# Performance work log

Hardware: AMD Instinct MI355X
Metric: run time of the kernel (lower is better)

## Reference

```python
import jax, jax.numpy as jnp
import numpy as np

HIDDEN = 1024
EMB = HIDDEN // 2          # embedding_dim = hidden_dim // 2
NUM_OPS = 8
BATCH = 16384


def setup_inputs() -> dict:
    key = jax.random.key(0)
    ks = jax.random.split(key, 8)
    x = jax.random.normal(ks[0], (BATCH, HIDDEN), dtype=jnp.float32)
    sampled_ops = jax.random.randint(ks[1], (BATCH,), 0, NUM_OPS, dtype=jnp.int32)
    op_emb = jax.random.normal(ks[2], (NUM_OPS, EMB), dtype=jnp.float32) * 0.02
    # per-expert 2-layer MLP params (Linear stored as [in, out] for x @ W)
    s1 = 1.0 / np.sqrt(HIDDEN + EMB)
    s2 = 1.0 / np.sqrt(HIDDEN)
    W1 = jax.random.uniform(ks[3], (NUM_OPS, HIDDEN + EMB, HIDDEN), jnp.float32, -s1, s1)
    b1 = jax.random.uniform(ks[4], (NUM_OPS, HIDDEN), jnp.float32, -s1, s1)
    W2 = jax.random.uniform(ks[5], (NUM_OPS, HIDDEN, HIDDEN), jnp.float32, -s2, s2)
    b2 = jax.random.uniform(ks[6], (NUM_OPS, HIDDEN), jnp.float32, -s2, s2)
    return {"x": x, "sampled_ops": sampled_ops, "op_emb": op_emb,
            "W1": W1, "b1": b1, "W2": W2, "b2": b2}


def reference(x, sampled_ops, op_emb, W1, b1, W2, b2):
    # gather per-token operator embedding and augment input
    emb = jnp.take(op_emb, sampled_ops, axis=0)            # [B, EMB]
    x_aug = jnp.concatenate([x, emb], axis=-1)             # [B, H+EMB]
    num_ops = W1.shape[0]
    out = jnp.zeros_like(x)
    # loop over the small fixed expert set; mask-combine per token
    for o in range(num_ops):
        h = jax.nn.relu(x_aug @ W1[o] + b1[o])             # [B, H]
        y = jax.nn.relu(h @ W2[o] + b2[o])                 # [B, H]
        mask = (sampled_ops == o)[:, None]
        out = out + jnp.where(mask, y, 0.0)
    return out
```

## Files before the change

kernel.cpp:

```cpp
#include <hip/hip_runtime.h>
#include <hip/hip_bf16.h>

#define BATCH 16384
#define HID   1024
#define EMBD  512
#define NOPS  8
#define MAXT  136
#define CNTS  16

typedef __attribute__((ext_vector_type(8))) short bf16x8;
typedef __attribute__((ext_vector_type(4))) float f32x4;

__device__ __forceinline__ unsigned short f2bf(float f) {
  unsigned int u = __float_as_uint(f);
  u += 0x7FFF + ((u >> 16) & 1);
  return (unsigned short)(u >> 16);
}

__device__ __forceinline__ unsigned int pk2(float a, float b) {
  __hip_bfloat162 t = __float22bfloat162_rn(make_float2(a, b));
  return *(unsigned int*)(&t);
}

__device__ __forceinline__ void lds_load16(void* lds, const void* g) {
  __builtin_amdgcn_global_load_lds(
      (const __attribute__((address_space(1))) unsigned int*)g,
      (__attribute__((address_space(3))) unsigned int*)lds, 16, 0, 0);
}

__device__ __forceinline__ void decode_bid(int bid, int& g, int& nx) {
  g = 17 * (bid & 7) + (bid >> 6);
  nx = (bid >> 3) & 7;
}

__device__ __forceinline__ void w_prep_tile(const float* __restrict__ W,
                                            short* __restrict__ Wp,
                                            int ks, int nx, int tid) {
  int n = tid & 127, kh = tid >> 7;
  const float* src = W + (size_t)(ks * 32 + kh * 16) * 1024 + nx * 128 + n;
  float v[16];
#pragma unroll
  for (int kk = 0; kk < 16; ++kk) v[kk] = src[(size_t)kk * 1024];
  uint4 a, b;
  a.x = pk2(v[0], v[1]);  a.y = pk2(v[2], v[3]);
  a.z = pk2(v[4], v[5]);  a.w = pk2(v[6], v[7]);
  b.x = pk2(v[8], v[9]);  b.y = pk2(v[10], v[11]);
  b.z = pk2(v[12], v[13]); b.w = pk2(v[14], v[15]);
  uint4* dst = (uint4*)(Wp + (size_t)n * 32);
  dst[kh * 2] = a;
  dst[kh * 2 + 1] = b;
}

__global__ void bucket_ce_k(const int* __restrict__ ops, int* __restrict__ cnt,
                            int* __restrict__ idx, const float* __restrict__ W1,
                            const float* __restrict__ emb,
                            const float* __restrict__ b1, float* __restrict__ ce) {
  int bid = blockIdx.x;
  int tid = threadIdx.x;
  if (bid < 128) {
    int e = bid >> 4, kp = bid & 15;
    int n = tid * 4;
    const float* Wc = W1 + (size_t)e * 1536 * 1024 + (size_t)(1024 + kp * 32) * 1024 + n;
    const float* ee = emb + e * EMBD + kp * 32;
    float4 a = make_float4(0.f, 0.f, 0.f, 0.f);
#pragma unroll
    for (int kk = 0; kk < 32; ++kk) {
      float s = ee[kk];
      float4 r = *(const float4*)(Wc + (size_t)kk * 1024);
      a.x += s * r.x; a.y += s * r.y; a.z += s * r.z; a.w += s * r.w;
    }
    if (kp == 0) {
      float4 b = *(const float4*)(b1 + e * HID + n);
      a.x += b.x; a.y += b.y; a.z += b.z; a.w += b.w;
    }
    float* d = ce + e * HID + n;
    atomicAdd(d + 0, a.x); atomicAdd(d + 1, a.y);
    atomicAdd(d + 2, a.z); atomicAdd(d + 3, a.w);
    return;
  }
  __shared__ int wcnt[4][NOPS];
  __shared__ int wbase[4][NOPS];
  int lane = tid & 63, w = tid >> 6;
  int t = (bid - 128) * 256 + tid;
  int op = ops[t];
  unsigned long long msave = 0;
#pragma unroll
  for (int o = 0; o < NOPS; ++o) {
    unsigned long long mm = __ballot(op == o);
    if (op == o) msave = mm;
    if (lane == o) wcnt[w][o] = __popcll(mm);
  }
  __syncthreads();
  if (tid < NOPS) {
    int c0 = wcnt[0][tid], c1 = wcnt[1][tid], c2 = wcnt[2][tid], c3 = wcnt[3][tid];
    int base = atomicAdd(&cnt[tid * CNTS], c0 + c1 + c2 + c3);
    wbase[0][tid] = base;
    wbase[1][tid] = base + c0;
    wbase[2][tid] = base + c0 + c1;
    wbase[3][tid] = base + c0 + c1 + c2;
  }
  __syncthreads();
  int pre = __popcll(msave & ((1ull << lane) - 1ull));
  idx[op * BATCH + wbase[w][op] + pre] = t;
}

__global__ void schedule_k(const int* __restrict__ cnt, int* __restrict__ desc,
                           int* __restrict__ ntp, int* __restrict__ idx) {
  if (threadIdx.x == 0) {
    int n = 0;
    for (int e = 0; e < NOPS; ++e) {
      int c = cnt[e * CNTS];
      for (int t = 0; t < c; t += 128) { desc[2 * n] = e; desc[2 * n + 1] = t; ++n; }
    }
    *ntp = n;
  }
  for (int e = 0; e < NOPS; ++e) {
    int c = cnt[e * CNTS];
    int cp = (c + 127) & ~127;
    for (int p = c + (int)threadIdx.x; p < cp; p += 256) idx[e * BATCH + p] = 0;
  }
}

__global__ void prep_k(const float* __restrict__ x,
                       const int* __restrict__ idx, const int* __restrict__ desc,
                       const int* __restrict__ ntp, short* __restrict__ Ap,
                       const float* __restrict__ W1, short* __restrict__ W1p) {
  int bid = blockIdx.x;
  int tid = threadIdx.x;
  if (bid >= 8 * MAXT) {
    int b = bid - 8 * MAXT;
    int e = b / 256; int r = b % 256; int nx = r / 32, ks = r % 32;
    w_prep_tile(W1 + (size_t)e * 1536 * 1024,
                W1p + ((size_t)(e * 8 + nx) * 32 + ks) * 4096, ks, nx, tid);
    return;
  }
  __shared__ int toks[128];
  int g = bid >> 3, kx = bid & 7;
  if (g >= *ntp) return;
  int e = desc[2 * g], rs = desc[2 * g + 1];
  if (tid < 128) toks[tid] = idx[e * BATCH + rs + tid];
  __syncthreads();
  int r = tid >> 1, ah = tid & 1;
  int tok = toks[r];
  short* dst0 = Ap + (size_t)g * 32 * 4096;
#pragma unroll
  for (int kk = 0; kk < 4; ++kk) {
    int ks = kx * 4 + kk;
    const float* src = x + (size_t)tok * HID + ks * 32 + ah * 16;
    float4 f0 = ((const float4*)src)[0];
    float4 f1 = ((const float4*)src)[1];
    float4 f2v = ((const float4*)src)[2];
    float4 f3 = ((const float4*)src)[3];
    uint4 p0 = make_uint4(pk2(f0.x, f0.y), pk2(f0.z, f0.w), pk2(f1.x, f1.y), pk2(f1.z, f1.w));
    uint4 p1 = make_uint4(pk2(f2v.x, f2v.y), pk2(f2v.z, f2v.w), pk2(f3.x, f3.y), pk2(f3.z, f3.w));
    short* dst = dst0 + ks * 4096 + r * 32 + ah * 16;
    ((uint4*)dst)[0] = p0;
    ((uint4*)dst)[1] = p1;
  }
}

__global__ __launch_bounds__(256) void gemm1_w2_k(
    const short* __restrict__ Ap, const float* __restrict__ ce,
    const short* __restrict__ W1p, unsigned short* __restrict__ hp,
    const int* __restrict__ desc, const int* __restrict__ ntp,
    const float* __restrict__ W2, short* __restrict__ W2p) {
  int bid = blockIdx.x;
  int tid = threadIdx.x;
  if (bid >= 8 * MAXT) {
    int b = bid - 8 * MAXT;
    int e = b / 256; int r = b % 256; int nx = r / 32, ks = r % 32;
    w_prep_tile(W2 + (size_t)e * 1024 * 1024,
                W2p + ((size_t)(e * 8 + nx) * 32 + ks) * 4096, ks, nx, tid);
    return;
  }
  int g, nx;
  decode_bid(bid, g, nx);
  if (g >= *ntp) return;
  int e = desc[2 * g];

  __shared__ __align__(16) char smem[16384];
  short* lA = (short*)smem;
  short* lB = (short*)(smem + 8192);

  int lane = tid & 63, w = tid >> 6;
  int wm = w >> 1, wn = w & 1;
  int fr = lane & 15, fq = lane >> 4;

  const char* Asrc = (const char*)Ap + (size_t)g * 32 * 8192;
  const char* Bsrc = (const char*)W1p + (size_t)(e * 8 + nx) * 32 * 8192;

  f32x4 acc[4][4] = {};

  for (int ks = 0; ks < 32; ++ks) {
    const char* as = Asrc + ks * 8192;
    const char* bs = Bsrc + ks * 8192;
    lds_load16(smem + w * 1024, as + w * 1024 + lane * 16);
    lds_load16(smem + 4096 + w * 1024, as + 4096 + w * 1024 + lane * 16);
    lds_load16(smem + 8192 + w * 1024, bs + w * 1024 + lane * 16);
    lds_load16(smem + 12288 + w * 1024, bs + 4096 + w * 1024 + lane * 16);
    __syncthreads();

    bf16x8 af[4], bfr[4];
#pragma unroll
    for (int i = 0; i < 4; ++i)
      af[i] = *(const bf16x8*)&lA[(wm * 64 + i * 16 + fr) * 32 + fq * 8];
#pragma unroll
    for (int j = 0; j < 4; ++j)
      bfr[j] = *(const bf16x8*)&lB[(wn * 64 + j * 16 + fr) * 32 + fq * 8];
#pragma unroll
    for (int i = 0; i < 4; ++i)
#pragma unroll
      for (int j = 0; j < 4; ++j)
        acc[i][j] = __builtin_amdgcn_mfma_f32_16x16x32_bf16(af[i], bfr[j], acc[i][j], 0, 0, 0);
    __syncthreads();
  }

  float bias[4];
#pragma unroll
  for (int j = 0; j < 4; ++j)
    bias[j] = ce[e * HID + nx * 128 + wn * 64 + j * 16 + fr];

  unsigned short* ls = (unsigned short*)smem;
  int lr = lane >> 2;
#pragma unroll
  for (int i = 0; i < 4; ++i) {
    __syncthreads();
#pragma unroll
    for (int j = 0; j < 4; ++j)
#pragma unroll
      for (int rg = 0; rg < 4; ++rg) {
        float v = acc[i][j][rg] + bias[j];
        v = v > 0.f ? v : 0.f;
        ls[w * 1024 + (fq * 4 + rg) * 64 + j * 16 + fr] = f2bf(v);
      }
    __syncthreads();
    int R = wm * 64 + i * 16 + lr;
#pragma unroll
    for (int s = 0; s < 2; ++s) {
      int ch = (lane & 3) + s * 4;
      int ks2 = nx * 4 + wn * 2 + (ch >> 2);
      uint4 val = *(const uint4*)&ls[w * 1024 + lr * 64 + ch * 8];
      *(uint4*)(hp + ((size_t)(g * 32 + ks2) * 128 + R) * 32 + (ch & 3) * 8) = val;
    }
  }
}

__global__ __launch_bounds__(256) void gemm2_k(
    const unsigned short* __restrict__ hp, const float* __restrict__ b2,
    const short* __restrict__ W2p, float* __restrict__ out,
    const int* __restrict__ idx, const int* __restrict__ cnt,
    const int* __restrict__ desc, const int* __restrict__ ntp) {
  int g, nx;
  decode_bid(blockIdx.x, g, nx);
  if (g >= *ntp) return;
  int e = desc[2 * g], rs = desc[2 * g + 1];
  int ce2 = cnt[e * CNTS];

  __shared__ __align__(16) char smem[16384];
  __shared__ int toks[128];
  short* lA = (short*)smem;
  short* lB = (short*)(smem + 8192);

  int tid = threadIdx.x, lane = tid & 63, w = tid >> 6;
  int wm = w >> 1, wn = w & 1;
  int fr = lane & 15, fq = lane >> 4;

  if (tid < 128) toks[tid] = idx[e * BATCH + rs + tid];

  const char* Asrc = (const char*)hp + (size_t)g * 32 * 8192;
  const char* Bsrc = (const char*)W2p + (size_t)(e * 8 + nx) * 32 * 8192;

  f32x4 acc[4][4] = {};

  for (int ks = 0; ks < 32; ++ks) {
    const char* as = Asrc + ks * 8192;
    const char* bs = Bsrc + ks * 8192;
    lds_load16(smem + w * 1024, as + w * 1024 + lane * 16);
    lds_load16(smem + 4096 + w * 1024, as + 4096 + w * 1024 + lane * 16);
    lds_load16(smem + 8192 + w * 1024, bs + w * 1024 + lane * 16);
    lds_load16(smem + 12288 + w * 1024, bs + 4096 + w * 1024 + lane * 16);
    __syncthreads();

    bf16x8 af[4], bfr[4];
#pragma unroll
    for (int i = 0; i < 4; ++i)
      af[i] = *(const bf16x8*)&lA[(wm * 64 + i * 16 + fr) * 32 + fq * 8];
#pragma unroll
    for (int j = 0; j < 4; ++j)
      bfr[j] = *(const bf16x8*)&lB[(wn * 64 + j * 16 + fr) * 32 + fq * 8];
#pragma unroll
    for (int i = 0; i < 4; ++i)
#pragma unroll
      for (int j = 0; j < 4; ++j)
        acc[i][j] = __builtin_amdgcn_mfma_f32_16x16x32_bf16(af[i], bfr[j], acc[i][j], 0, 0, 0);
    __syncthreads();
  }

  float bias[4];
#pragma unroll
  for (int j = 0; j < 4; ++j)
    bias[j] = b2[e * HID + nx * 128 + wn * 64 + j * 16 + fr];

  float* lsf = (float*)smem;
  int lr = lane >> 2;
#pragma unroll
  for (int i = 0; i < 4; ++i) {
    __syncthreads();
#pragma unroll
    for (int j = 0; j < 4; ++j)
#pragma unroll
      for (int rg = 0; rg < 4; ++rg) {
        float v = acc[i][j][rg] + bias[j];
        lsf[w * 1024 + (fq * 4 + rg) * 64 + j * 16 + fr] = v > 0.f ? v : 0.f;
      }
    __syncthreads();
    int R = wm * 64 + i * 16 + lr;
    if (R < ce2 - rs) {
      float* orow = out + (size_t)toks[R] * HID + nx * 128 + wn * 64;
#pragma unroll
      for (int s = 0; s < 4; ++s) {
        int ch = (lane & 3) + s * 4;
        *(float4*)(orow + ch * 4) = *(const float4*)&lsf[w * 1024 + lr * 64 + ch * 4];
      }
    }
  }
}


extern "C" void kernel_launch(void* const* d_in, const int* in_sizes, int n_in,
                              void* d_out, int out_size, void* d_ws, size_t ws_size,
                              hipStream_t stream) {
  const float* x   = (const float*)d_in[0];
  const int*   ops = (const int*)d_in[1];
  const float* emb = (const float*)d_in[2];
  const float* W1  = (const float*)d_in[3];
  const float* b1  = (const float*)d_in[4];
  const float* W2  = (const float*)d_in[5];
  const float* b2  = (const float*)d_in[6];
  float* out = (float*)d_out;

  char* ws = (char*)d_ws;
  int* cnt  = (int*)(ws + 0);
  float* ce = (float*)(ws + 512);
  int* ntp  = (int*)(ws + 33280);
  int* desc = (int*)(ws + 33344);
  int* idx  = (int*)(ws + 36864);
  short* W1p = (short*)(ws + 561152);
  short* W2p = (short*)(ws + 17338368);
  unsigned short* hp = (unsigned short*)(ws + 34115584);
  short* Ap = (short*)(ws + 69767168);

  hipMemsetAsync(ws, 0, 33280, stream);
  bucket_ce_k<<<128 + 64, 256, 0, stream>>>(ops, cnt, idx, W1, emb, b1, ce);
  schedule_k<<<1, 256, 0, stream>>>(cnt, desc, ntp, idx);
  prep_k<<<8 * MAXT + 2048, 256, 0, stream>>>(x, idx, desc, ntp, Ap, W1, W1p);
  gemm1_w2_k<<<8 * MAXT + 2048, 256, 0, stream>>>(Ap, ce, W1p, hp, desc, ntp, W2, W2p);
  gemm2_k<<<8 * MAXT, 256, 0, stream>>>(hp, b2, W2p, out, idx, cnt, desc, ntp);
}
```

Before: 303.4 us.

## Fuse token gather and bf16 conversion into GEMM1, drop prep kernel

Removes the separate prep kernel that gathered x rows and wrote a packed bf16 A buffer. GEMM1 now loads the gathered fp32 rows directly, converts them in registers and stores them to LDS, prefetching the next k-slice. W1 packing moves into the bucketing kernel. The packed tile layout changes to a k-quarter-major form, and the epilogue LDS staging gets an XOR swizzle to cut bank conflicts. Schedule descriptor writes are parallelised across threads. Each of the 8 column blocks now re-reads and re-converts the same x rows, which adds redundant global traffic and conversion work.

```diff
diff --git a/kernel.cpp b/kernel.cpp
--- a/kernel.cpp
+++ b/kernel.cpp
@@ -46,19 +46,28 @@
   a.z = pk2(v[4], v[5]);  a.w = pk2(v[6], v[7]);
   b.x = pk2(v[8], v[9]);  b.y = pk2(v[10], v[11]);
   b.z = pk2(v[12], v[13]); b.w = pk2(v[14], v[15]);
-  uint4* dst = (uint4*)(Wp + (size_t)n * 32);
-  dst[kh * 2] = a;
-  dst[kh * 2 + 1] = b;
+  uint4* dst = (uint4*)Wp;
+  dst[(2 * kh) * 128 + n]     = a;
+  dst[(2 * kh + 1) * 128 + n] = b;
 }
 
 __global__ void bucket_ce_k(const int* __restrict__ ops, int* __restrict__ cnt,
                             int* __restrict__ idx, const float* __restrict__ W1,
                             const float* __restrict__ emb,
-                            const float* __restrict__ b1, float* __restrict__ ce) {
+                            const float* __restrict__ b1, float* __restrict__ ce,
+                            short* __restrict__ W1p) {
   int bid = blockIdx.x;
   int tid = threadIdx.x;
-  if (bid < 128) {
-    int e = bid >> 4, kp = bid & 15;
+  if (bid >= 192) {
+    int b = bid - 192;
+    int e = b / 256; int rr = b % 256; int nx = rr / 32, ks = rr % 32;
+    w_prep_tile(W1 + (size_t)e * 1536 * 1024,
+                W1p + ((size_t)(e * 8 + nx) * 32 + ks) * 4096, ks, nx, tid);
+    return;
+  }
+  if (bid >= 64) {
+    int cb = bid - 64;
+    int e = cb >> 4, kp = cb & 15;
     int n = tid * 4;
     const float* Wc = W1 + (size_t)e * 1536 * 1024 + (size_t)(1024 + kp * 32) * 1024 + n;
     const float* ee = emb + e * EMBD + kp * 32;
@@ -81,7 +90,7 @@
   __shared__ int wcnt[4][NOPS];
   __shared__ int wbase[4][NOPS];
   int lane = tid & 63, w = tid >> 6;
-  int t = (bid - 128) * 256 + tid;
+  int t = bid * 256 + tid;
   int op = ops[t];
   unsigned long long msave = 0;
 #pragma unroll
@@ -106,69 +115,40 @@
 
 __global__ void schedule_k(const int* __restrict__ cnt, int* __restrict__ desc,
                            int* __restrict__ ntp, int* __restrict__ idx) {
-  if (threadIdx.x == 0) {
+  __shared__ int base[NOPS + 1];
+  int tid = threadIdx.x;
+  if (tid == 0) {
     int n = 0;
-    for (int e = 0; e < NOPS; ++e) {
-      int c = cnt[e * CNTS];
-      for (int t = 0; t < c; t += 128) { desc[2 * n] = e; desc[2 * n + 1] = t; ++n; }
-    }
+    for (int e = 0; e < NOPS; ++e) { base[e] = n; n += (cnt[e * CNTS] + 127) >> 7; }
+    base[NOPS] = n;
     *ntp = n;
+  }
+  __syncthreads();
+  for (int e = 0; e < NOPS; ++e) {
+    int b0 = base[e], nt = base[e + 1] - b0;
+    for (int t = tid; t < nt; t += 256) {
+      desc[2 * (b0 + t)] = e;
+      desc[2 * (b0 + t) + 1] = t * 128;
+    }
   }
   for (int e = 0; e < NOPS; ++e) {
     int c = cnt[e * CNTS];
     int cp = (c + 127) & ~127;
-    for (int p = c + (int)threadIdx.x; p < cp; p += 256) idx[e * BATCH + p] = 0;
-  }
-}
-
-__global__ void prep_k(const float* __restrict__ x,
-                       const int* __restrict__ idx, const int* __restrict__ desc,
-                       const int* __restrict__ ntp, short* __restrict__ Ap,
-                       const float* __restrict__ W1, short* __restrict__ W1p) {
+    for (int p = c + tid; p < cp; p += 256) idx[e * BATCH + p] = 0;
+  }
+}
+
+__global__ __launch_bounds__(256) void gemm1_w2_k(
+    const float* __restrict__ x, const int* __restrict__ idx,
+    const float* __restrict__ ce, const short* __restrict__ W1p,
+    unsigned short* __restrict__ hp, const int* __restrict__ desc,
+    const int* __restrict__ ntp, const float* __restrict__ W2,
+    short* __restrict__ W2p) {
   int bid = blockIdx.x;
   int tid = threadIdx.x;
   if (bid >= 8 * MAXT) {
     int b = bid - 8 * MAXT;
-    int e = b / 256; int r = b % 256; int nx = r / 32, ks = r % 32;
-    w_prep_tile(W1 + (size_t)e * 1536 * 1024,
-                W1p + ((size_t)(e * 8 + nx) * 32 + ks) * 4096, ks, nx, tid);
-    return;
-  }
-  __shared__ int toks[128];
-  int g = bid >> 3, kx = bid & 7;
-  if (g >= *ntp) return;
-  int e = desc[2 * g], rs = desc[2 * g + 1];
-  if (tid < 128) toks[tid] = idx[e * BATCH + rs + tid];
-  __syncthreads();
-  int r = tid >> 1, ah = tid & 1;
-  int tok = toks[r];
-  short* dst0 = Ap + (size_t)g * 32 * 4096;
-#pragma unroll
-  for (int kk = 0; kk < 4; ++kk) {
-    int ks = kx * 4 + kk;
-    const float* src = x + (size_t)tok * HID + ks * 32 + ah * 16;
-    float4 f0 = ((const float4*)src)[0];
-    float4 f1 = ((const float4*)src)[1];
-    float4 f2v = ((const float4*)src)[2];
-    float4 f3 = ((const float4*)src)[3];
-    uint4 p0 = make_uint4(pk2(f0.x, f0.y), pk2(f0.z, f0.w), pk2(f1.x, f1.y), pk2(f1.z, f1.w));
-    uint4 p1 = make_uint4(pk2(f2v.x, f2v.y), pk2(f2v.z, f2v.w), pk2(f3.x, f3.y), pk2(f3.z, f3.w));
-    short* dst = dst0 + ks * 4096 + r * 32 + ah * 16;
-    ((uint4*)dst)[0] = p0;
-    ((uint4*)dst)[1] = p1;
-  }
-}
-
-__global__ __launch_bounds__(256) void gemm1_w2_k(
-    const short* __restrict__ Ap, const float* __restrict__ ce,
-    const short* __restrict__ W1p, unsigned short* __restrict__ hp,
-    const int* __restrict__ desc, const int* __restrict__ ntp,
-    const float* __restrict__ W2, short* __restrict__ W2p) {
-  int bid = blockIdx.x;
-  int tid = threadIdx.x;
-  if (bid >= 8 * MAXT) {
-    int b = bid - 8 * MAXT;
-    int e = b / 256; int r = b % 256; int nx = r / 32, ks = r % 32;
+    int e = b / 256; int rr = b % 256; int nx = rr / 32, ks = rr % 32;
     w_prep_tile(W2 + (size_t)e * 1024 * 1024,
                 W2p + ((size_t)(e * 8 + nx) * 32 + ks) * 4096, ks, nx, tid);
     return;
@@ -176,37 +156,51 @@
   int g, nx;
   decode_bid(bid, g, nx);
   if (g >= *ntp) return;
-  int e = desc[2 * g];
+  int e = desc[2 * g], rs = desc[2 * g + 1];
 
   __shared__ __align__(16) char smem[16384];
+  __shared__ int toks[128];
   short* lA = (short*)smem;
   short* lB = (short*)(smem + 8192);
 
   int lane = tid & 63, w = tid >> 6;
   int wm = w >> 1, wn = w & 1;
   int fr = lane & 15, fq = lane >> 4;
-
-  const char* Asrc = (const char*)Ap + (size_t)g * 32 * 8192;
+  int ar = tid >> 1, ah = tid & 1;
+
+  if (tid < 128) toks[tid] = idx[e * BATCH + rs + tid];
+  __syncthreads();
+  const float* xrow = x + (size_t)toks[ar] * HID + ah * 16;
   const char* Bsrc = (const char*)W1p + (size_t)(e * 8 + nx) * 32 * 8192;
 
   f32x4 acc[4][4] = {};
+  float4 fa0 = ((const float4*)xrow)[0];
+  float4 fa1 = ((const float4*)xrow)[1];
+  float4 fa2 = ((const float4*)xrow)[2];
+  float4 fa3 = ((const float4*)xrow)[3];
 
   for (int ks = 0; ks < 32; ++ks) {
-    const char* as = Asrc + ks * 8192;
     const char* bs = Bsrc + ks * 8192;
-    lds_load16(smem + w * 1024, as + w * 1024 + lane * 16);
-    lds_load16(smem + 4096 + w * 1024, as + 4096 + w * 1024 + lane * 16);
     lds_load16(smem + 8192 + w * 1024, bs + w * 1024 + lane * 16);
     lds_load16(smem + 12288 + w * 1024, bs + 4096 + w * 1024 + lane * 16);
-    __syncthreads();
-
+    uint4 p0 = make_uint4(pk2(fa0.x, fa0.y), pk2(fa0.z, fa0.w),
+                          pk2(fa1.x, fa1.y), pk2(fa1.z, fa1.w));
+    uint4 p1 = make_uint4(pk2(fa2.x, fa2.y), pk2(fa2.z, fa2.w),
+                          pk2(fa3.x, fa3.y), pk2(fa3.z, fa3.w));
+    *(uint4*)&lA[((2 * ah) * 128 + ar) * 8] = p0;
+    *(uint4*)&lA[((2 * ah + 1) * 128 + ar) * 8] = p1;
+    __syncthreads();
+    if (ks < 31) {
+      const float4* src = (const float4*)(xrow + (ks + 1) * 32);
+      fa0 = src[0]; fa1 = src[1]; fa2 = src[2]; fa3 = src[3];
+    }
     bf16x8 af[4], bfr[4];
 #pragma unroll
     for (int i = 0; i < 4; ++i)
-      af[i] = *(const bf16x8*)&lA[(wm * 64 + i * 16 + fr) * 32 + fq * 8];
+      af[i] = *(const bf16x8*)&lA[(fq * 128 + wm * 64 + i * 16 + fr) * 8];
 #pragma unroll
     for (int j = 0; j < 4; ++j)
-      bfr[j] = *(const bf16x8*)&lB[(wn * 64 + j * 16 + fr) * 32 + fq * 8];
+      bfr[j] = *(const bf16x8*)&lB[(fq * 128 + wn * 64 + j * 16 + fr) * 8];
 #pragma unroll
     for (int i = 0; i < 4; ++i)
 #pragma unroll
@@ -220,7 +214,6 @@
   for (int j = 0; j < 4; ++j)
     bias[j] = ce[e * HID + nx * 128 + wn * 64 + j * 16 + fr];
 
-  unsigned short* ls = (unsigned short*)smem;
   int lr = lane >> 2;
 #pragma unroll
   for (int i = 0; i < 4; ++i) {
@@ -231,16 +224,22 @@
       for (int rg = 0; rg < 4; ++rg) {
         float v = acc[i][j][rg] + bias[j];
         v = v > 0.f ? v : 0.f;
-        ls[w * 1024 + (fq * 4 + rg) * 64 + j * 16 + fr] = f2bf(v);
+        int row16 = fq * 4 + rg;
+        int off = w * 2048 + row16 * 128 + (j * 16 + fr) * 2;
+        off ^= (row16 & 1) << 6;
+        *(unsigned short*)(smem + off) = f2bf(v);
       }
     __syncthreads();
     int R = wm * 64 + i * 16 + lr;
 #pragma unroll
     for (int s = 0; s < 2; ++s) {
       int ch = (lane & 3) + s * 4;
+      int off = w * 2048 + lr * 128 + ch * 16;
+      off ^= (lr & 1) << 6;
+      uint4 val = *(const uint4*)(smem + off);
       int ks2 = nx * 4 + wn * 2 + (ch >> 2);
-      uint4 val = *(const uint4*)&ls[w * 1024 + lr * 64 + ch * 8];
-      *(uint4*)(hp + ((size_t)(g * 32 + ks2) * 128 + R) * 32 + (ch & 3) * 8) = val;
+      int kq = ch & 3;
+      *(uint4*)(hp + (((size_t)(g * 32 + ks2) * 4 + kq) * 128 + R) * 8) = val;
     }
   }
 }
@@ -284,10 +283,10 @@
     bf16x8 af[4], bfr[4];
 #pragma unroll
     for (int i = 0; i < 4; ++i)
-      af[i] = *(const bf16x8*)&lA[(wm * 64 + i * 16 + fr) * 32 + fq * 8];
+      af[i] = *(const bf16x8*)&lA[(fq * 128 + wm * 64 + i * 16 + fr) * 8];
 #pragma unroll
     for (int j = 0; j < 4; ++j)
-      bfr[j] = *(const bf16x8*)&lB[(wn * 64 + j * 16 + fr) * 32 + fq * 8];
+      bfr[j] = *(const bf16x8*)&lB[(fq * 128 + wn * 64 + j * 16 + fr) * 8];
 #pragma unroll
     for (int i = 0; i < 4; ++i)
 #pragma unroll
@@ -301,7 +300,6 @@
   for (int j = 0; j < 4; ++j)
     bias[j] = b2[e * HID + nx * 128 + wn * 64 + j * 16 + fr];
 
-  float* lsf = (float*)smem;
   int lr = lane >> 2;
 #pragma unroll
   for (int i = 0; i < 4; ++i) {
@@ -311,7 +309,10 @@
 #pragma unroll
       for (int rg = 0; rg < 4; ++rg) {
         float v = acc[i][j][rg] + bias[j];
-        lsf[w * 1024 + (fq * 4 + rg) * 64 + j * 16 + fr] = v > 0.f ? v : 0.f;
+        int row16 = fq * 4 + rg;
+        int off = w * 4096 + row16 * 256 + (j * 16 + fr) * 4;
+        off ^= (row16 & 1) << 6;
+        *(float*)(smem + off) = v > 0.f ? v : 0.f;
       }
     __syncthreads();
     int R = wm * 64 + i * 16 + lr;
@@ -320,7 +321,9 @@
 #pragma unroll
       for (int s = 0; s < 4; ++s) {
         int ch = (lane & 3) + s * 4;
-        *(float4*)(orow + ch * 4) = *(const float4*)&lsf[w * 1024 + lr * 64 + ch * 4];
+        int off = w * 4096 + lr * 256 + ch * 16;
+        off ^= (lr & 1) << 6;
+        *(float4*)(orow + ch * 4) = *(const float4*)(smem + off);
       }
     }
   }
@@ -348,12 +351,10 @@
   short* W1p = (short*)(ws + 561152);
   short* W2p = (short*)(ws + 17338368);
   unsigned short* hp = (unsigned short*)(ws + 34115584);
-  short* Ap = (short*)(ws + 69767168);
 
   hipMemsetAsync(ws, 0, 33280, stream);
-  bucket_ce_k<<<128 + 64, 256, 0, stream>>>(ops, cnt, idx, W1, emb, b1, ce);
+  bucket_ce_k<<<192 + 2048, 256, 0, stream>>>(ops, cnt, idx, W1, emb, b1, ce, W1p);
   schedule_k<<<1, 256, 0, stream>>>(cnt, desc, ntp, idx);
-  prep_k<<<8 * MAXT + 2048, 256, 0, stream>>>(x, idx, desc, ntp, Ap, W1, W1p);
-  gemm1_w2_k<<<8 * MAXT + 2048, 256, 0, stream>>>(Ap, ce, W1p, hp, desc, ntp, W2, W2p);
+  gemm1_w2_k<<<8 * MAXT + 2048, 256, 0, stream>>>(x, idx, ce, W1p, hp, desc, ntp, W2, W2p);
   gemm2_k<<<8 * MAXT, 256, 0, stream>>>(hp, b2, W2p, out, idx, cnt, desc, ntp);
 }
```

Result: slower. 324.4 us (+6.9%).
